# Performance work log

Hardware: AMD Instinct MI355X
Metric: run time of the kernel (lower is better)

## Reference

```python
import jax, jax.numpy as jnp
import numpy as np

ATOM_FDIM = 35
BOND_FDIM = 5
MAX_NB = 10
HIDDEN = 128
DEPTH = 6
A = 131072   # total atoms
B = 262144   # total directed bonds
M = 32768    # tree messages (row 0 is the zero pad vector, as in the torch code)
N_MOLS = 4096


def setup_inputs() -> dict:
    key = jax.random.key(0)
    ks = jax.random.split(key, 9)
    atom_feats = jax.random.uniform(ks[0], (A, ATOM_FDIM), dtype=jnp.float32)
    bond_feats = jax.random.uniform(ks[1], (B, ATOM_FDIM + BOND_FDIM), dtype=jnp.float32)
    tree_message = jax.random.normal(ks[2], (M, HIDDEN), dtype=jnp.float32)
    tree_message = tree_message.at[0].set(0.0)  # all_mess[0] = zeros padding
    atom_graph = jax.random.randint(ks[3], (A, MAX_NB), 0, M + B)
    bond_graph = jax.random.randint(ks[4], (B, MAX_NB), 0, M + B)
    s = 1.0 / np.sqrt(HIDDEN)
    W_i = jax.random.uniform(ks[5], (HIDDEN, ATOM_FDIM + BOND_FDIM), jnp.float32, -s, s)
    W_h = jax.random.uniform(ks[6], (HIDDEN, HIDDEN), jnp.float32, -s, s)
    W_o = jax.random.uniform(ks[7], (HIDDEN, ATOM_FDIM + HIDDEN), jnp.float32, -s, s)
    b_o = jax.random.uniform(ks[8], (HIDDEN,), jnp.float32, -s, s)
    return {"atom_feats": atom_feats, "bond_feats": bond_feats,
            "tree_message": tree_message, "atom_graph": atom_graph,
            "bond_graph": bond_graph, "n_mols": N_MOLS,
            "W_i": W_i, "W_h": W_h, "W_o": W_o, "b_o": b_o}


def reference(atom_feats, bond_feats, tree_message, atom_graph, bond_graph,
              n_mols, W_i, W_h, W_o, b_o):
    # h0 = ReLU(W_i @ bond_feats): [B, H]
    h0 = jax.nn.relu(jnp.einsum('bf,hf->bh', bond_feats, W_i))
    graph_message = h0
    for _ in range(DEPTH - 1):
        message = jnp.concatenate([tree_message, graph_message], axis=0)  # [M+B, H]
        nei = jnp.take(message, bond_graph, axis=0).sum(axis=1)           # [B, H]
        graph_message = jax.nn.relu(h0 + jnp.einsum('bh,gh->bg', nei, W_h))
    message = jnp.concatenate([tree_message, graph_message], axis=0)
    nei_a = jnp.take(message, atom_graph, axis=0).sum(axis=1)             # [A, H]
    atom_in = jnp.concatenate([atom_feats, nei_a], axis=1)                # [A, F+H]
    atom_hiddens = jax.nn.relu(jnp.einsum('af,hf->ah', atom_in, W_o) + b_o)
    # per-molecule mean over equal-size contiguous scopes
    atoms_per_mol = A // n_mols
    mol_ids = jnp.arange(A) // atoms_per_mol
    mol_vecs = jax.ops.segment_sum(atom_hiddens, mol_ids, num_segments=n_mols)
    return mol_vecs / atoms_per_mol
```

## Files before the change

### kernel.cpp

```cpp
#include <hip/hip_runtime.h>

#define H       128
#define MAXNB   10
#define M_TREE  32768
#define NBOND   262144
#define NATOM   131072
#define FATOM   35
#define FBOND   40
#define FOUT    163
#define KPAD    192
#define NMOLS   4096
#define APM     32
#define TB      64
#define TA      64

typedef __bf16 bf16x8 __attribute__((ext_vector_type(8)));
typedef float  f32x4  __attribute__((ext_vector_type(4)));
typedef unsigned int u32x4 __attribute__((ext_vector_type(4)));
typedef unsigned int u32x2 __attribute__((ext_vector_type(2)));

__device__ __forceinline__ unsigned short f32_to_bf16(float f) {
  unsigned int u = __float_as_uint(f);
  u += 0x7FFFu + ((u >> 16) & 1u);
  return (unsigned short)(u >> 16);
}
__device__ __forceinline__ float bf16u_to_f32(unsigned short h) {
  return __uint_as_float(((unsigned int)h) << 16);
}
__device__ __forceinline__ unsigned int bfpair_addrelu(unsigned int a, unsigned int h) {
  float a0 = __uint_as_float(a << 16), a1 = __uint_as_float(a & 0xFFFF0000u);
  float h0v = __uint_as_float(h << 16), h1v = __uint_as_float(h & 0xFFFF0000u);
  float r0 = fmaxf(a0 + h0v, 0.f), r1 = fmaxf(a1 + h1v, 0.f);
  return ((unsigned int)f32_to_bf16(r1) << 16) | (unsigned int)f32_to_bf16(r0);
}

__global__ __launch_bounds__(256) void prep(const float* __restrict__ tm,
                                            const float* __restrict__ wh,
                                            const float* __restrict__ wo,
                                            const float* __restrict__ wi,
                                            unsigned short* __restrict__ tmsg,
                                            unsigned short* __restrict__ whb,
                                            unsigned short* __restrict__ wob,
                                            unsigned short* __restrict__ wib) {
  const int blk = blockIdx.x;
  if (blk < 4096) {
    int i = (blk * 256 + threadIdx.x) * 4;
    f32x4 v = __builtin_nontemporal_load((const f32x4*)(tm + i));
    u32x2 p;
    p.x = (unsigned int)f32_to_bf16(v.x) | ((unsigned int)f32_to_bf16(v.y) << 16);
    p.y = (unsigned int)f32_to_bf16(v.z) | ((unsigned int)f32_to_bf16(v.w) << 16);
    *(u32x2*)(tmsg + i) = p;
    return;
  }
  int j = (blk - 4096) * 256 + threadIdx.x;
  const int n2 = H * H;
  const int n3 = H * KPAD;
  const int n4 = H * 64;
  if (j < n2) { whb[j] = f32_to_bf16(wh[j]); return; }
  int k = j - n2;
  if (k < n3) {
    int g = k / KPAD, kk = k - g * KPAD;
    float v = 0.f;
    if (kk < 35)                   v = wo[g * FOUT + kk];
    else if (kk >= 36 && kk < 164) v = wo[g * FOUT + kk - 1];
    wob[k] = f32_to_bf16(v);
    return;
  }
  int m = k - n3;
  if (m < n4) {
    int g = m / 64, kk = m - g * 64;
    wib[m] = (kk < FBOND) ? f32_to_bf16(wi[g * FBOND + kk]) : (unsigned short)0;
  }
}

__global__ __launch_bounds__(256, 3) void wi_gemm(const float* __restrict__ bond_feats,
                                                  const unsigned short* __restrict__ wib,
                                                  unsigned short* __restrict__ h0) {
  __shared__ unsigned short sF[128][72];
  const int t = threadIdx.x;
  const int lane = t & 63;
  const int wave = t >> 6;
  const int n16 = lane & 15;
  const int quad = lane >> 4;
  const int b0 = blockIdx.x * 128;

#pragma unroll
  for (int c = 0; c < 5; ++c) {
    int q = c * 256 + t;
    f32x4 v = __builtin_nontemporal_load((const f32x4*)(bond_feats + (size_t)b0 * FBOND + q * 4));
    int flat = q * 4;
    int row = flat / 40, col = flat - row * 40;
    u32x2 p;
    p.x = (unsigned int)f32_to_bf16(v.x) | ((unsigned int)f32_to_bf16(v.y) << 16);
    p.y = (unsigned int)f32_to_bf16(v.z) | ((unsigned int)f32_to_bf16(v.w) << 16);
    *(u32x2*)&sF[row][col] = p;
  }
  for (int i = t; i < 128 * 24; i += 256) {
    int b = i / 24, c = 40 + i - b * 24;
    sF[b][c] = 0;
  }
  bf16x8 Bf[2][2];
#pragma unroll
  for (int kt = 0; kt < 2; ++kt)
#pragma unroll
    for (int nt = 0; nt < 2; ++nt)
      Bf[kt][nt] = *(const bf16x8*)(wib + ((wave * 2 + nt) * 16 + n16) * 64 + kt * 32 + quad * 8);
  __syncthreads();

  f32x4 acc[8][2];
  f32x4 zero = {0.f, 0.f, 0.f, 0.f};
#pragma unroll
  for (int mt = 0; mt < 8; ++mt) { acc[mt][0] = zero; acc[mt][1] = zero; }
#pragma unroll
  for (int kt = 0; kt < 2; ++kt)
#pragma unroll
    for (int mt = 0; mt < 8; ++mt) {
      bf16x8 av = *(const bf16x8*)&sF[mt * 16 + n16][kt * 32 + quad * 8];
      acc[mt][0] = __builtin_amdgcn_mfma_f32_16x16x32_bf16(av, Bf[kt][0], acc[mt][0], 0, 0, 0);
      acc[mt][1] = __builtin_amdgcn_mfma_f32_16x16x32_bf16(av, Bf[kt][1], acc[mt][1], 0, 0, 0);
    }
#pragma unroll
  for (int mt = 0; mt < 8; ++mt)
#pragma unroll
    for (int nt = 0; nt < 2; ++nt) {
      const int col = (wave * 2 + nt) * 16 + n16;
#pragma unroll
      for (int r = 0; r < 4; ++r) {
        const int b = b0 + mt * 16 + quad * 4 + r;
        h0[b * H + col] = f32_to_bf16(fmaxf(acc[mt][nt][r], 0.f));
      }
    }
}

__global__ __launch_bounds__(256, 6) void mp_step(const unsigned short* __restrict__ gm_in,
                                                  unsigned short* __restrict__ gm_out,
                                                  const unsigned short* __restrict__ h0,
                                                  const unsigned short* __restrict__ tmsg,
                                                  const int* __restrict__ bond_graph,
                                                  const unsigned short* __restrict__ whb) {
  __shared__ unsigned short snei[TB][136];
  __shared__ int sBG[TB * MAXNB];
  const int t = threadIdx.x;
  const int lane = t & 63;
  const int wave = t >> 6;
  const int n16 = lane & 15;
  const int quad = lane >> 4;
  const int b0 = blockIdx.x * TB;

  for (int i = t; i < TB * MAXNB; i += 256) sBG[i] = bond_graph[b0 * MAXNB + i];
  __syncthreads();

  const unsigned short* gsh = gm_in - (size_t)M_TREE * H;
  for (int lb = wave * 4; lb < TB; lb += 16) {
    unsigned int u[4][MAXNB];
#pragma unroll
    for (int p = 0; p < 4; ++p) {
      const int* ig = &sBG[(lb + p) * MAXNB];
#pragma unroll
      for (int j = 0; j < MAXNB; ++j) {
        int idx = __builtin_amdgcn_readfirstlane(ig[j]);
        const unsigned short* r = ((idx < M_TREE) ? tmsg : gsh) + (size_t)idx * H;
        u[p][j] = *(const unsigned int*)(r + 2 * lane);
      }
    }
#pragma unroll
    for (int p = 0; p < 4; ++p) {
      float a0 = 0.f, a1 = 0.f;
#pragma unroll
      for (int j = 0; j < MAXNB; ++j) {
        a0 += __uint_as_float(u[p][j] << 16);
        a1 += __uint_as_float(u[p][j] & 0xFFFF0000u);
      }
      unsigned int packed = ((unsigned int)f32_to_bf16(a1) << 16) | (unsigned int)f32_to_bf16(a0);
      *(unsigned int*)&snei[lb + p][2 * lane] = packed;
    }
  }

  bf16x8 Bf[4][2];
#pragma unroll
  for (int kt = 0; kt < 4; ++kt)
#pragma unroll
    for (int nt = 0; nt < 2; ++nt)
      Bf[kt][nt] = *(const bf16x8*)(whb + ((wave * 2 + nt) * 16 + n16) * H + kt * 32 + quad * 8);
  __syncthreads();

  f32x4 acc[4][2];
  f32x4 zero = {0.f, 0.f, 0.f, 0.f};
#pragma unroll
  for (int mt = 0; mt < 4; ++mt) { acc[mt][0] = zero; acc[mt][1] = zero; }
#pragma unroll
  for (int kt = 0; kt < 4; ++kt)
#pragma unroll
    for (int mt = 0; mt < 4; ++mt) {
      bf16x8 av = *(const bf16x8*)&snei[mt * 16 + n16][kt * 32 + quad * 8];
      acc[mt][0] = __builtin_amdgcn_mfma_f32_16x16x32_bf16(av, Bf[kt][0], acc[mt][0], 0, 0, 0);
      acc[mt][1] = __builtin_amdgcn_mfma_f32_16x16x32_bf16(av, Bf[kt][1], acc[mt][1], 0, 0, 0);
    }
  __syncthreads();

#pragma unroll
  for (int mt = 0; mt < 4; ++mt)
#pragma unroll
    for (int nt = 0; nt < 2; ++nt) {
      const int col = (wave * 2 + nt) * 16 + n16;
#pragma unroll
      for (int r = 0; r < 4; ++r)
        snei[mt * 16 + quad * 4 + r][col] = f32_to_bf16(acc[mt][nt][r]);
    }
  __syncthreads();

  const size_t gbase = (size_t)b0 * H;
#pragma unroll
  for (int c = 0; c < 4; ++c) {
    int fl = c * 256 + t;
    int row = fl >> 4;
    int col = (fl & 15) * 8;
    u32x4 a4 = *(const u32x4*)&snei[row][col];
    u32x4 h4 = *(const u32x4*)(h0 + gbase + (size_t)row * H + col);
    u32x4 o4;
    o4.x = bfpair_addrelu(a4.x, h4.x);
    o4.y = bfpair_addrelu(a4.y, h4.y);
    o4.z = bfpair_addrelu(a4.z, h4.z);
    o4.w = bfpair_addrelu(a4.w, h4.w);
    *(u32x4*)(gm_out + gbase + (size_t)row * H + col) = o4;
  }
}

__global__ __launch_bounds__(256, 5) void readout(const float* __restrict__ atom_feats,
                                                  const unsigned short* __restrict__ gm,
                                                  const unsigned short* __restrict__ tmsg,
                                                  const int* __restrict__ atom_graph,
                                                  const unsigned short* __restrict__ wob,
                                                  const float* __restrict__ b_o,
                                                  float* __restrict__ out) {
  __shared__ unsigned short sA[TA][200];
  __shared__ int sAG[TA * MAXNB];
  const int t = threadIdx.x;
  const int lane = t & 63;
  const int wave = t >> 6;
  const int n16 = lane & 15;
  const int quad = lane >> 4;
  const int blk = blockIdx.x;
  const int abase = blk * TA;

  for (int i = t; i < TA * MAXNB; i += 256)
    sAG[i] = __builtin_nontemporal_load(atom_graph + abase * MAXNB + i);
  for (int i = t; i < TA * FATOM; i += 256) {
    int a = i / FATOM, f = i - a * FATOM;
    sA[a][f] = f32_to_bf16(__builtin_nontemporal_load(atom_feats + abase * FATOM + i));
  }
  if (t < TA) sA[t][35] = 0;
  for (int i = t; i < TA * 28; i += 256) {
    int a = i / 28, c = 164 + i - a * 28;
    sA[a][c] = 0;
  }
  __syncthreads();

  const unsigned short* gsh = gm - (size_t)M_TREE * H;
  for (int la = wave * 2; la < TA; la += 8) {
    unsigned int u[2][MAXNB];
#pragma unroll
    for (int p = 0; p < 2; ++p) {
      const int* ig = &sAG[(la + p) * MAXNB];
#pragma unroll
      for (int j = 0; j < MAXNB; ++j) {
        int idx = __builtin_amdgcn_readfirstlane(ig[j]);
        const unsigned short* r = ((idx < M_TREE) ? tmsg : gsh) + (size_t)idx * H;
        u[p][j] = *(const unsigned int*)(r + 2 * lane);
      }
    }
#pragma unroll
    for (int p = 0; p < 2; ++p) {
      float a0 = 0.f, a1 = 0.f;
#pragma unroll
      for (int j = 0; j < MAXNB; ++j) {
        a0 += __uint_as_float(u[p][j] << 16);
        a1 += __uint_as_float(u[p][j] & 0xFFFF0000u);
      }
      unsigned int packed = ((unsigned int)f32_to_bf16(a1) << 16) | (unsigned int)f32_to_bf16(a0);
      *(unsigned int*)&sA[la + p][36 + 2 * lane] = packed;
    }
  }

  bf16x8 Bf[6][2];
#pragma unroll
  for (int kt = 0; kt < 6; ++kt)
#pragma unroll
    for (int nt = 0; nt < 2; ++nt)
      Bf[kt][nt] = *(const bf16x8*)(wob + ((wave * 2 + nt) * 16 + n16) * KPAD + kt * 32 + quad * 8);
  __syncthreads();

  f32x4 acc[4][2];
  f32x4 zero = {0.f, 0.f, 0.f, 0.f};
#pragma unroll
  for (int mt = 0; mt < 4; ++mt) { acc[mt][0] = zero; acc[mt][1] = zero; }
#pragma unroll
  for (int kt = 0; kt < 6; ++kt)
#pragma unroll
    for (int mt = 0; mt < 4; ++mt) {
      bf16x8 av = *(const bf16x8*)&sA[mt * 16 + n16][kt * 32 + quad * 8];
      acc[mt][0] = __builtin_amdgcn_mfma_f32_16x16x32_bf16(av, Bf[kt][0], acc[mt][0], 0, 0, 0);
      acc[mt][1] = __builtin_amdgcn_mfma_f32_16x16x32_bf16(av, Bf[kt][1], acc[mt][1], 0, 0, 0);
    }

  float bo[2] = { b_o[(wave * 2) * 16 + n16], b_o[(wave * 2 + 1) * 16 + n16] };
  float part[2][2] = {{0.f,0.f},{0.f,0.f}};
#pragma unroll
  for (int mt = 0; mt < 4; ++mt)
#pragma unroll
    for (int nt = 0; nt < 2; ++nt)
#pragma unroll
      for (int r = 0; r < 4; ++r)
        part[mt >> 1][nt] += fmaxf(acc[mt][nt][r] + bo[nt], 0.f);
#pragma unroll
  for (int mol = 0; mol < 2; ++mol)
#pragma unroll
    for (int nt = 0; nt < 2; ++nt) {
      float p = part[mol][nt];
      p += __shfl_xor(p, 16);
      p += __shfl_xor(p, 32);
      if (lane < 16)
        out[(blk * 2 + mol) * H + (wave * 2 + nt) * 16 + lane] = p * (1.0f / APM);
    }
}

extern "C" void kernel_launch(void* const* d_in, const int* in_sizes, int n_in,
                              void* d_out, int out_size, void* d_ws, size_t ws_size,
                              hipStream_t stream) {
  (void)in_sizes; (void)n_in; (void)out_size; (void)ws_size;
  const float* atom_feats   = (const float*)d_in[0];
  const float* bond_feats   = (const float*)d_in[1];
  const float* tree_message = (const float*)d_in[2];
  const int*   atom_graph   = (const int*)d_in[3];
  const int*   bond_graph   = (const int*)d_in[4];
  const float* W_i = (const float*)d_in[6];
  const float* W_h = (const float*)d_in[7];
  const float* W_o = (const float*)d_in[8];
  const float* b_o = (const float*)d_in[9];
  float* out = (float*)d_out;

  char* ws = (char*)d_ws;
  unsigned short* tmsg = (unsigned short*)(ws);
  unsigned short* whb  = (unsigned short*)(ws + 8388608);
  unsigned short* wob  = (unsigned short*)(ws + 8421376);
  unsigned short* wib  = (unsigned short*)(ws + 8470528);
  unsigned short* h0   = (unsigned short*)(ws + 8486912);
  unsigned short* gm0  = (unsigned short*)(ws + 75595776);
  unsigned short* gm1  = (unsigned short*)(ws + 142704640);

  prep<<<4288, 256, 0, stream>>>(tree_message, W_h, W_o, W_i, tmsg, whb, wob, wib);
  wi_gemm<<<NBOND / 128, 256, 0, stream>>>(bond_feats, wib, h0);
  mp_step<<<NBOND / TB, 256, 0, stream>>>(h0,  gm0, h0, tmsg, bond_graph, whb);
  mp_step<<<NBOND / TB, 256, 0, stream>>>(gm0, gm1, h0, tmsg, bond_graph, whb);
  mp_step<<<NBOND / TB, 256, 0, stream>>>(gm1, gm0, h0, tmsg, bond_graph, whb);
  mp_step<<<NBOND / TB, 256, 0, stream>>>(gm0, gm1, h0, tmsg, bond_graph, whb);
  mp_step<<<NBOND / TB, 256, 0, stream>>>(gm1, gm0, h0, tmsg, bond_graph, whb);
  readout<<<NATOM / TA, 256, 0, stream>>>(atom_feats, gm0, tmsg, atom_graph, wob, b_o, out);
}
```

Measured before the change: 747.2 us.

## Precompute constant tree-message term once and gather only graph messages per step

The W_h product is linear, so the tree-message part of the neighbour sum never changes across steps. It is now computed once inside wi_gemm and folded with h0 into a precomputed bias (hT). Each message-passing step then gathers only graph messages: a remapped bond_graph sends every tree index to a zeroed pad row, which removes the per-neighbour tree/graph pointer select and the scattered tree-row reads. Nontemporal loads and stores are added for streamed buffers. The cost is an extra bf16 rounding of the folded bias, an extra index-remap pass in prep, and more work in wi_gemm.

New measurement: 812.6 us. +8.8%, slower.

```diff
diff --git a/kernel.cpp b/kernel.cpp
--- a/kernel.cpp
+++ b/kernel.cpp
@@ -18,6 +18,7 @@
 typedef float  f32x4  __attribute__((ext_vector_type(4)));
 typedef unsigned int u32x4 __attribute__((ext_vector_type(4)));
 typedef unsigned int u32x2 __attribute__((ext_vector_type(2)));
+typedef int          i32x4 __attribute__((ext_vector_type(4)));
 
 __device__ __forceinline__ unsigned short f32_to_bf16(float f) {
   unsigned int u = __float_as_uint(f);
@@ -38,10 +39,14 @@
                                             const float* __restrict__ wh,
                                             const float* __restrict__ wo,
                                             const float* __restrict__ wi,
+                                            const int* __restrict__ bond_graph,
                                             unsigned short* __restrict__ tmsg,
                                             unsigned short* __restrict__ whb,
                                             unsigned short* __restrict__ wob,
-                                            unsigned short* __restrict__ wib) {
+                                            unsigned short* __restrict__ wib,
+                                            int* __restrict__ bg2,
+                                            unsigned short* __restrict__ bufA,
+                                            unsigned short* __restrict__ gm0) {
   const int blk = blockIdx.x;
   if (blk < 4096) {
     int i = (blk * 256 + threadIdx.x) * 4;
@@ -52,31 +57,54 @@
     *(u32x2*)(tmsg + i) = p;
     return;
   }
-  int j = (blk - 4096) * 256 + threadIdx.x;
-  const int n2 = H * H;
-  const int n3 = H * KPAD;
-  const int n4 = H * 64;
-  if (j < n2) { whb[j] = f32_to_bf16(wh[j]); return; }
-  int k = j - n2;
-  if (k < n3) {
-    int g = k / KPAD, kk = k - g * KPAD;
-    float v = 0.f;
-    if (kk < 35)                   v = wo[g * FOUT + kk];
-    else if (kk >= 36 && kk < 164) v = wo[g * FOUT + kk - 1];
-    wob[k] = f32_to_bf16(v);
+  if (blk < 4288) {
+    int j = (blk - 4096) * 256 + threadIdx.x;
+    const int n2 = H * H;
+    const int n3 = H * KPAD;
+    const int n4 = H * 64;
+    if (j < n2) { whb[j] = f32_to_bf16(wh[j]); return; }
+    int k = j - n2;
+    if (k < n3) {
+      int g = k / KPAD, kk = k - g * KPAD;
+      float v = 0.f;
+      if (kk < 35)                   v = wo[g * FOUT + kk];
+      else if (kk >= 36 && kk < 164) v = wo[g * FOUT + kk - 1];
+      wob[k] = f32_to_bf16(v);
+      return;
+    }
+    int m = k - n3;
+    if (m < n4) {
+      int g = m / 64, kk = m - g * 64;
+      wib[m] = (kk < FBOND) ? f32_to_bf16(wi[g * FBOND + kk]) : (unsigned short)0;
+    }
     return;
   }
-  int m = k - n3;
-  if (m < n4) {
-    int g = m / 64, kk = m - g * 64;
-    wib[m] = (kk < FBOND) ? f32_to_bf16(wi[g * FBOND + kk]) : (unsigned short)0;
+  if (blk < 4288 + 2560) {
+    int q = ((blk - 4288) * 256 + threadIdx.x) * 4;
+    i32x4 v = __builtin_nontemporal_load((const i32x4*)(bond_graph + q));
+    i32x4 o;
+    o.x = (v.x < M_TREE) ? NBOND : (v.x - M_TREE);
+    o.y = (v.y < M_TREE) ? NBOND : (v.y - M_TREE);
+    o.z = (v.z < M_TREE) ? NBOND : (v.z - M_TREE);
+    o.w = (v.w < M_TREE) ? NBOND : (v.w - M_TREE);
+    __builtin_nontemporal_store(o, (i32x4*)(bg2 + q));
+    return;
+  }
+  if (threadIdx.x < 128) {
+    bufA[(size_t)NBOND * H + threadIdx.x] = 0;
+    gm0 [(size_t)NBOND * H + threadIdx.x] = 0;
   }
 }
 
 __global__ __launch_bounds__(256, 3) void wi_gemm(const float* __restrict__ bond_feats,
                                                   const unsigned short* __restrict__ wib,
-                                                  unsigned short* __restrict__ h0) {
-  __shared__ unsigned short sF[128][72];
+                                                  const unsigned short* __restrict__ whb,
+                                                  const unsigned short* __restrict__ tmsg,
+                                                  const int* __restrict__ bond_graph,
+                                                  unsigned short* __restrict__ h0,
+                                                  unsigned short* __restrict__ hT) {
+  __shared__ unsigned short sT[128][136];
+  __shared__ int sBG[128 * MAXNB];
   const int t = threadIdx.x;
   const int lane = t & 63;
   const int wave = t >> 6;
@@ -93,18 +121,21 @@
     u32x2 p;
     p.x = (unsigned int)f32_to_bf16(v.x) | ((unsigned int)f32_to_bf16(v.y) << 16);
     p.y = (unsigned int)f32_to_bf16(v.z) | ((unsigned int)f32_to_bf16(v.w) << 16);
-    *(u32x2*)&sF[row][col] = p;
+    *(u32x2*)&sT[row][col] = p;
   }
   for (int i = t; i < 128 * 24; i += 256) {
     int b = i / 24, c = 40 + i - b * 24;
-    sF[b][c] = 0;
-  }
-  bf16x8 Bf[2][2];
+    sT[b][c] = 0;
+  }
+  for (int i = t; i < 128 * MAXNB; i += 256)
+    sBG[i] = __builtin_nontemporal_load(bond_graph + (size_t)b0 * MAXNB + i);
+
+  bf16x8 Bi[2][2];
 #pragma unroll
   for (int kt = 0; kt < 2; ++kt)
 #pragma unroll
     for (int nt = 0; nt < 2; ++nt)
-      Bf[kt][nt] = *(const bf16x8*)(wib + ((wave * 2 + nt) * 16 + n16) * 64 + kt * 32 + quad * 8);
+      Bi[kt][nt] = *(const bf16x8*)(wib + ((wave * 2 + nt) * 16 + n16) * 64 + kt * 32 + quad * 8);
   __syncthreads();
 
   f32x4 acc[8][2];
@@ -115,9 +146,9 @@
   for (int kt = 0; kt < 2; ++kt)
 #pragma unroll
     for (int mt = 0; mt < 8; ++mt) {
-      bf16x8 av = *(const bf16x8*)&sF[mt * 16 + n16][kt * 32 + quad * 8];
-      acc[mt][0] = __builtin_amdgcn_mfma_f32_16x16x32_bf16(av, Bf[kt][0], acc[mt][0], 0, 0, 0);
-      acc[mt][1] = __builtin_amdgcn_mfma_f32_16x16x32_bf16(av, Bf[kt][1], acc[mt][1], 0, 0, 0);
+      bf16x8 av = *(const bf16x8*)&sT[mt * 16 + n16][kt * 32 + quad * 8];
+      acc[mt][0] = __builtin_amdgcn_mfma_f32_16x16x32_bf16(av, Bi[kt][0], acc[mt][0], 0, 0, 0);
+      acc[mt][1] = __builtin_amdgcn_mfma_f32_16x16x32_bf16(av, Bi[kt][1], acc[mt][1], 0, 0, 0);
     }
 #pragma unroll
   for (int mt = 0; mt < 8; ++mt)
@@ -127,16 +158,64 @@
 #pragma unroll
       for (int r = 0; r < 4; ++r) {
         const int b = b0 + mt * 16 + quad * 4 + r;
-        h0[b * H + col] = f32_to_bf16(fmaxf(acc[mt][nt][r], 0.f));
-      }
-    }
+        __builtin_nontemporal_store(f32_to_bf16(fmaxf(acc[mt][nt][r], 0.f)), &h0[(size_t)b * H + col]);
+      }
+    }
+  __syncthreads();
+
+  for (int lb = wave * 4; lb < 128; lb += 16) {
+#pragma unroll
+    for (int p = 0; p < 4; ++p) {
+      const int* ig = &sBG[(lb + p) * MAXNB];
+      float a0 = 0.f, a1 = 0.f;
+#pragma unroll
+      for (int j = 0; j < MAXNB; ++j) {
+        int idx = __builtin_amdgcn_readfirstlane(ig[j]);
+        if (idx < M_TREE) {
+          unsigned int u = *(const unsigned int*)(tmsg + (size_t)idx * H + 2 * lane);
+          a0 += __uint_as_float(u << 16);
+          a1 += __uint_as_float(u & 0xFFFF0000u);
+        }
+      }
+      unsigned int packed = ((unsigned int)f32_to_bf16(a1) << 16) | (unsigned int)f32_to_bf16(a0);
+      *(unsigned int*)&sT[lb + p][2 * lane] = packed;
+    }
+  }
+
+  bf16x8 Bh[4][2];
+#pragma unroll
+  for (int kt = 0; kt < 4; ++kt)
+#pragma unroll
+    for (int nt = 0; nt < 2; ++nt)
+      Bh[kt][nt] = *(const bf16x8*)(whb + ((wave * 2 + nt) * 16 + n16) * H + kt * 32 + quad * 8);
+  __syncthreads();
+
+#pragma unroll
+  for (int mt = 0; mt < 8; ++mt) {
+    f32x4 acch[2] = {zero, zero};
+#pragma unroll
+    for (int kt = 0; kt < 4; ++kt) {
+      bf16x8 av = *(const bf16x8*)&sT[mt * 16 + n16][kt * 32 + quad * 8];
+      acch[0] = __builtin_amdgcn_mfma_f32_16x16x32_bf16(av, Bh[kt][0], acch[0], 0, 0, 0);
+      acch[1] = __builtin_amdgcn_mfma_f32_16x16x32_bf16(av, Bh[kt][1], acch[1], 0, 0, 0);
+    }
+#pragma unroll
+    for (int nt = 0; nt < 2; ++nt) {
+      const int col = (wave * 2 + nt) * 16 + n16;
+#pragma unroll
+      for (int r = 0; r < 4; ++r) {
+        const int b = b0 + mt * 16 + quad * 4 + r;
+        float hr = fmaxf(acc[mt][nt][r], 0.f);
+        __builtin_nontemporal_store(f32_to_bf16(hr + acch[nt][r]), &hT[(size_t)b * H + col]);
+      }
+    }
+  }
 }
 
 __global__ __launch_bounds__(256, 6) void mp_step(const unsigned short* __restrict__ gm_in,
                                                   unsigned short* __restrict__ gm_out,
-                                                  const unsigned short* __restrict__ h0,
-                                                  const unsigned short* __restrict__ tmsg,
-                                                  const int* __restrict__ bond_graph,
+                                                  const unsigned short* __restrict__ hT,
+                                                  const int* __restrict__ bg2,
                                                   const unsigned short* __restrict__ whb) {
   __shared__ unsigned short snei[TB][136];
   __shared__ int sBG[TB * MAXNB];
@@ -147,10 +226,10 @@
   const int quad = lane >> 4;
   const int b0 = blockIdx.x * TB;
 
-  for (int i = t; i < TB * MAXNB; i += 256) sBG[i] = bond_graph[b0 * MAXNB + i];
-  __syncthreads();
-
-  const unsigned short* gsh = gm_in - (size_t)M_TREE * H;
+  for (int i = t; i < TB * MAXNB; i += 256)
+    sBG[i] = __builtin_nontemporal_load(bg2 + (size_t)b0 * MAXNB + i);
+  __syncthreads();
+
   for (int lb = wave * 4; lb < TB; lb += 16) {
     unsigned int u[4][MAXNB];
 #pragma unroll
@@ -159,8 +238,7 @@
 #pragma unroll
       for (int j = 0; j < MAXNB; ++j) {
         int idx = __builtin_amdgcn_readfirstlane(ig[j]);
-        const unsigned short* r = ((idx < M_TREE) ? tmsg : gsh) + (size_t)idx * H;
-        u[p][j] = *(const unsigned int*)(r + 2 * lane);
+        u[p][j] = *(const unsigned int*)(gm_in + (size_t)idx * H + 2 * lane);
       }
     }
 #pragma unroll
@@ -216,13 +294,13 @@
     int row = fl >> 4;
     int col = (fl & 15) * 8;
     u32x4 a4 = *(const u32x4*)&snei[row][col];
-    u32x4 h4 = *(const u32x4*)(h0 + gbase + (size_t)row * H + col);
+    u32x4 h4 = __builtin_nontemporal_load((const u32x4*)(hT + gbase + (size_t)row * H + col));
     u32x4 o4;
     o4.x = bfpair_addrelu(a4.x, h4.x);
     o4.y = bfpair_addrelu(a4.y, h4.y);
     o4.z = bfpair_addrelu(a4.z, h4.z);
     o4.w = bfpair_addrelu(a4.w, h4.w);
-    *(u32x4*)(gm_out + gbase + (size_t)row * H + col) = o4;
+    __builtin_nontemporal_store(o4, (u32x4*)(gm_out + gbase + (size_t)row * H + col));
   }
 }
 
@@ -344,16 +422,18 @@
   unsigned short* whb  = (unsigned short*)(ws + 8388608);
   unsigned short* wob  = (unsigned short*)(ws + 8421376);
   unsigned short* wib  = (unsigned short*)(ws + 8470528);
-  unsigned short* h0   = (unsigned short*)(ws + 8486912);
-  unsigned short* gm0  = (unsigned short*)(ws + 75595776);
-  unsigned short* gm1  = (unsigned short*)(ws + 142704640);
-
-  prep<<<4288, 256, 0, stream>>>(tree_message, W_h, W_o, W_i, tmsg, whb, wob, wib);
-  wi_gemm<<<NBOND / 128, 256, 0, stream>>>(bond_feats, wib, h0);
-  mp_step<<<NBOND / TB, 256, 0, stream>>>(h0,  gm0, h0, tmsg, bond_graph, whb);
-  mp_step<<<NBOND / TB, 256, 0, stream>>>(gm0, gm1, h0, tmsg, bond_graph, whb);
-  mp_step<<<NBOND / TB, 256, 0, stream>>>(gm1, gm0, h0, tmsg, bond_graph, whb);
-  mp_step<<<NBOND / TB, 256, 0, stream>>>(gm0, gm1, h0, tmsg, bond_graph, whb);
-  mp_step<<<NBOND / TB, 256, 0, stream>>>(gm1, gm0, h0, tmsg, bond_graph, whb);
+  int*            bg2  = (int*)           (ws + 8486912);
+  unsigned short* bufA = (unsigned short*)(ws + 18972672);
+  unsigned short* gm0  = (unsigned short*)(ws + 86081792);
+  unsigned short* hT   = (unsigned short*)(ws + 153190912);
+
+  prep<<<6849, 256, 0, stream>>>(tree_message, W_h, W_o, W_i, bond_graph,
+                                 tmsg, whb, wob, wib, bg2, bufA, gm0);
+  wi_gemm<<<NBOND / 128, 256, 0, stream>>>(bond_feats, wib, whb, tmsg, bond_graph, bufA, hT);
+  mp_step<<<NBOND / TB, 256, 0, stream>>>(bufA, gm0, hT, bg2, whb);
+  mp_step<<<NBOND / TB, 256, 0, stream>>>(gm0, bufA, hT, bg2, whb);
+  mp_step<<<NBOND / TB, 256, 0, stream>>>(bufA, gm0, hT, bg2, whb);
+  mp_step<<<NBOND / TB, 256, 0, stream>>>(gm0, bufA, hT, bg2, whb);
+  mp_step<<<NBOND / TB, 256, 0, stream>>>(bufA, gm0, hT, bg2, whb);
   readout<<<NATOM / TA, 256, 0, stream>>>(atom_feats, gm0, tmsg, atom_graph, wob, b_o, out);
 }
```

## Use contiguous tree+graph message buffers with 16-byte vector gathers and dot2 accumulation

Applied to the files above, without the earlier changes.

Stores the tree messages in front of each ping-pong graph message buffer, so a single base pointer indexes the concatenated message table and the per-neighbor tmsg/gm branch and readfirstlane go away. Each gather now has 16 lanes per bond loading 16-byte chunks, with 4 bonds per wave instruction, instead of one bond per wave with 4-byte loads. Accumulation switches to v_dot2_f32_bf16. In exchange, the tree messages are written twice and h0 is duplicated into the A buffer, and the readout padding layout is shifted to align columns to 8.

Result: no change. 753.7 us (+0.9%).

```diff
diff --git a/kernel.cpp b/kernel.cpp
--- a/kernel.cpp
+++ b/kernel.cpp
@@ -9,7 +9,6 @@
 #define FBOND   40
 #define FOUT    163
 #define KPAD    192
-#define NMOLS   4096
 #define APM     32
 #define TB      64
 #define TA      64
@@ -18,14 +17,13 @@
 typedef float  f32x4  __attribute__((ext_vector_type(4)));
 typedef unsigned int u32x4 __attribute__((ext_vector_type(4)));
 typedef unsigned int u32x2 __attribute__((ext_vector_type(2)));
+typedef int          i32x4 __attribute__((ext_vector_type(4)));
+typedef int          i32x2 __attribute__((ext_vector_type(2)));
 
 __device__ __forceinline__ unsigned short f32_to_bf16(float f) {
   unsigned int u = __float_as_uint(f);
   u += 0x7FFFu + ((u >> 16) & 1u);
   return (unsigned short)(u >> 16);
-}
-__device__ __forceinline__ float bf16u_to_f32(unsigned short h) {
-  return __uint_as_float(((unsigned int)h) << 16);
 }
 __device__ __forceinline__ unsigned int bfpair_addrelu(unsigned int a, unsigned int h) {
   float a0 = __uint_as_float(a << 16), a1 = __uint_as_float(a & 0xFFFF0000u);
@@ -33,12 +31,20 @@
   float r0 = fmaxf(a0 + h0v, 0.f), r1 = fmaxf(a1 + h1v, 0.f);
   return ((unsigned int)f32_to_bf16(r1) << 16) | (unsigned int)f32_to_bf16(r0);
 }
+__device__ __forceinline__ void bfdot_acc(unsigned int u, float& a0, float& a1) {
+  asm("v_dot2_f32_bf16 %0, %1, %2, %0" : "+v"(a0) : "v"(u), "v"(0x00003F80u));
+  asm("v_dot2_f32_bf16 %0, %1, %2, %0" : "+v"(a1) : "v"(u), "v"(0x3F800000u));
+}
+__device__ __forceinline__ unsigned int pack2(float a0, float a1) {
+  return ((unsigned int)f32_to_bf16(a1) << 16) | (unsigned int)f32_to_bf16(a0);
+}
 
 __global__ __launch_bounds__(256) void prep(const float* __restrict__ tm,
                                             const float* __restrict__ wh,
                                             const float* __restrict__ wo,
                                             const float* __restrict__ wi,
-                                            unsigned short* __restrict__ tmsg,
+                                            unsigned short* __restrict__ tA,
+                                            unsigned short* __restrict__ tB,
                                             unsigned short* __restrict__ whb,
                                             unsigned short* __restrict__ wob,
                                             unsigned short* __restrict__ wib) {
@@ -49,7 +55,8 @@
     u32x2 p;
     p.x = (unsigned int)f32_to_bf16(v.x) | ((unsigned int)f32_to_bf16(v.y) << 16);
     p.y = (unsigned int)f32_to_bf16(v.z) | ((unsigned int)f32_to_bf16(v.w) << 16);
-    *(u32x2*)(tmsg + i) = p;
+    *(u32x2*)(tA + i) = p;
+    *(u32x2*)(tB + i) = p;
     return;
   }
   int j = (blk - 4096) * 256 + threadIdx.x;
@@ -62,7 +69,7 @@
     int g = k / KPAD, kk = k - g * KPAD;
     float v = 0.f;
     if (kk < 35)                   v = wo[g * FOUT + kk];
-    else if (kk >= 36 && kk < 164) v = wo[g * FOUT + kk - 1];
+    else if (kk >= 40 && kk < 168) v = wo[g * FOUT + kk - 5];
     wob[k] = f32_to_bf16(v);
     return;
   }
@@ -75,7 +82,8 @@
 
 __global__ __launch_bounds__(256, 3) void wi_gemm(const float* __restrict__ bond_feats,
                                                   const unsigned short* __restrict__ wib,
-                                                  unsigned short* __restrict__ h0) {
+                                                  unsigned short* __restrict__ h0,
+                                                  unsigned short* __restrict__ h0A) {
   __shared__ unsigned short sF[128][72];
   const int t = threadIdx.x;
   const int lane = t & 63;
@@ -127,19 +135,20 @@
 #pragma unroll
       for (int r = 0; r < 4; ++r) {
         const int b = b0 + mt * 16 + quad * 4 + r;
-        h0[b * H + col] = f32_to_bf16(fmaxf(acc[mt][nt][r], 0.f));
+        unsigned short hv = f32_to_bf16(fmaxf(acc[mt][nt][r], 0.f));
+        h0 [(size_t)b * H + col] = hv;
+        h0A[(size_t)b * H + col] = hv;
       }
     }
 }
 
-__global__ __launch_bounds__(256, 6) void mp_step(const unsigned short* __restrict__ gm_in,
+__global__ __launch_bounds__(256, 6) void mp_step(const unsigned short* __restrict__ src,
                                                   unsigned short* __restrict__ gm_out,
                                                   const unsigned short* __restrict__ h0,
-                                                  const unsigned short* __restrict__ tmsg,
                                                   const int* __restrict__ bond_graph,
                                                   const unsigned short* __restrict__ whb) {
   __shared__ unsigned short snei[TB][136];
-  __shared__ int sBG[TB * MAXNB];
+  __shared__ int sBG[TB][16];
   const int t = threadIdx.x;
   const int lane = t & 63;
   const int wave = t >> 6;
@@ -147,33 +156,42 @@
   const int quad = lane >> 4;
   const int b0 = blockIdx.x * TB;
 
-  for (int i = t; i < TB * MAXNB; i += 256) sBG[i] = bond_graph[b0 * MAXNB + i];
-  __syncthreads();
-
-  const unsigned short* gsh = gm_in - (size_t)M_TREE * H;
-  for (int lb = wave * 4; lb < TB; lb += 16) {
-    unsigned int u[4][MAXNB];
-#pragma unroll
-    for (int p = 0; p < 4; ++p) {
-      const int* ig = &sBG[(lb + p) * MAXNB];
-#pragma unroll
-      for (int j = 0; j < MAXNB; ++j) {
-        int idx = __builtin_amdgcn_readfirstlane(ig[j]);
-        const unsigned short* r = ((idx < M_TREE) ? tmsg : gsh) + (size_t)idx * H;
-        u[p][j] = *(const unsigned int*)(r + 2 * lane);
-      }
-    }
-#pragma unroll
-    for (int p = 0; p < 4; ++p) {
-      float a0 = 0.f, a1 = 0.f;
-#pragma unroll
-      for (int j = 0; j < MAXNB; ++j) {
-        a0 += __uint_as_float(u[p][j] << 16);
-        a1 += __uint_as_float(u[p][j] & 0xFFFF0000u);
-      }
-      unsigned int packed = ((unsigned int)f32_to_bf16(a1) << 16) | (unsigned int)f32_to_bf16(a0);
-      *(unsigned int*)&snei[lb + p][2 * lane] = packed;
-    }
+  for (int i = t; i < TB * MAXNB; i += 256) {
+    int b = i / MAXNB, j = i - b * MAXNB;
+    sBG[b][j] = bond_graph[(size_t)b0 * MAXNB + i];
+  }
+  __syncthreads();
+
+  const unsigned char* sp = (const unsigned char*)src;
+  const unsigned int so = (unsigned int)n16 * 16u;
+  for (int it = 0; it < 4; ++it) {
+    const int lb = wave * 16 + it * 4 + quad;
+    i32x4 iv0 = *(const i32x4*)&sBG[lb][0];
+    i32x4 iv1 = *(const i32x4*)&sBG[lb][4];
+    i32x2 iv2 = *(const i32x2*)&sBG[lb][8];
+    unsigned int ix[10] = {(unsigned int)iv0.x, (unsigned int)iv0.y, (unsigned int)iv0.z,
+                           (unsigned int)iv0.w, (unsigned int)iv1.x, (unsigned int)iv1.y,
+                           (unsigned int)iv1.z, (unsigned int)iv1.w, (unsigned int)iv2.x,
+                           (unsigned int)iv2.y};
+    u32x4 u4[10];
+#pragma unroll
+    for (int j = 0; j < MAXNB; ++j)
+      u4[j] = *(const u32x4*)(sp + (ix[j] * 256u + so));
+    float ac0 = 0.f, ac1 = 0.f, ac2 = 0.f, ac3 = 0.f;
+    float ac4 = 0.f, ac5 = 0.f, ac6 = 0.f, ac7 = 0.f;
+#pragma unroll
+    for (int j = 0; j < MAXNB; ++j) {
+      bfdot_acc(u4[j].x, ac0, ac1);
+      bfdot_acc(u4[j].y, ac2, ac3);
+      bfdot_acc(u4[j].z, ac4, ac5);
+      bfdot_acc(u4[j].w, ac6, ac7);
+    }
+    u32x4 o;
+    o.x = pack2(ac0, ac1);
+    o.y = pack2(ac2, ac3);
+    o.z = pack2(ac4, ac5);
+    o.w = pack2(ac6, ac7);
+    *(u32x4*)&snei[lb][n16 * 8] = o;
   }
 
   bf16x8 Bf[4][2];
@@ -227,14 +245,13 @@
 }
 
 __global__ __launch_bounds__(256, 5) void readout(const float* __restrict__ atom_feats,
-                                                  const unsigned short* __restrict__ gm,
-                                                  const unsigned short* __restrict__ tmsg,
+                                                  const unsigned short* __restrict__ src,
                                                   const int* __restrict__ atom_graph,
                                                   const unsigned short* __restrict__ wob,
                                                   const float* __restrict__ b_o,
                                                   float* __restrict__ out) {
-  __shared__ unsigned short sA[TA][200];
-  __shared__ int sAG[TA * MAXNB];
+  __shared__ unsigned short sA[TA][208];
+  __shared__ int sAG[TA][16];
   const int t = threadIdx.x;
   const int lane = t & 63;
   const int wave = t >> 6;
@@ -243,43 +260,54 @@
   const int blk = blockIdx.x;
   const int abase = blk * TA;
 
-  for (int i = t; i < TA * MAXNB; i += 256)
-    sAG[i] = __builtin_nontemporal_load(atom_graph + abase * MAXNB + i);
+  for (int i = t; i < TA * MAXNB; i += 256) {
+    int a = i / MAXNB, j = i - a * MAXNB;
+    sAG[a][j] = __builtin_nontemporal_load(atom_graph + (size_t)abase * MAXNB + i);
+  }
   for (int i = t; i < TA * FATOM; i += 256) {
     int a = i / FATOM, f = i - a * FATOM;
-    sA[a][f] = f32_to_bf16(__builtin_nontemporal_load(atom_feats + abase * FATOM + i));
-  }
-  if (t < TA) sA[t][35] = 0;
-  for (int i = t; i < TA * 28; i += 256) {
-    int a = i / 28, c = 164 + i - a * 28;
+    sA[a][f] = f32_to_bf16(__builtin_nontemporal_load(atom_feats + (size_t)abase * FATOM + i));
+  }
+  if (t < TA) {
+#pragma unroll
+    for (int c = 35; c < 40; ++c) sA[t][c] = 0;
+  }
+  for (int i = t; i < TA * 24; i += 256) {
+    int a = i / 24, c = 168 + i - a * 24;
     sA[a][c] = 0;
   }
   __syncthreads();
 
-  const unsigned short* gsh = gm - (size_t)M_TREE * H;
-  for (int la = wave * 2; la < TA; la += 8) {
-    unsigned int u[2][MAXNB];
-#pragma unroll
-    for (int p = 0; p < 2; ++p) {
-      const int* ig = &sAG[(la + p) * MAXNB];
-#pragma unroll
-      for (int j = 0; j < MAXNB; ++j) {
-        int idx = __builtin_amdgcn_readfirstlane(ig[j]);
-        const unsigned short* r = ((idx < M_TREE) ? tmsg : gsh) + (size_t)idx * H;
-        u[p][j] = *(const unsigned int*)(r + 2 * lane);
-      }
-    }
-#pragma unroll
-    for (int p = 0; p < 2; ++p) {
-      float a0 = 0.f, a1 = 0.f;
-#pragma unroll
-      for (int j = 0; j < MAXNB; ++j) {
-        a0 += __uint_as_float(u[p][j] << 16);
-        a1 += __uint_as_float(u[p][j] & 0xFFFF0000u);
-      }
-      unsigned int packed = ((unsigned int)f32_to_bf16(a1) << 16) | (unsigned int)f32_to_bf16(a0);
-      *(unsigned int*)&sA[la + p][36 + 2 * lane] = packed;
-    }
+  const unsigned char* sp = (const unsigned char*)src;
+  const unsigned int so = (unsigned int)n16 * 16u;
+  for (int it = 0; it < 4; ++it) {
+    const int la = wave * 16 + it * 4 + quad;
+    i32x4 iv0 = *(const i32x4*)&sAG[la][0];
+    i32x4 iv1 = *(const i32x4*)&sAG[la][4];
+    i32x2 iv2 = *(const i32x2*)&sAG[la][8];
+    unsigned int ix[10] = {(unsigned int)iv0.x, (unsigned int)iv0.y, (unsigned int)iv0.z,
+                           (unsigned int)iv0.w, (unsigned int)iv1.x, (unsigned int)iv1.y,
+                           (unsigned int)iv1.z, (unsigned int)iv1.w, (unsigned int)iv2.x,
+                           (unsigned int)iv2.y};
+    u32x4 u4[10];
+#pragma unroll
+    for (int j = 0; j < MAXNB; ++j)
+      u4[j] = *(const u32x4*)(sp + (ix[j] * 256u + so));
+    float ac0 = 0.f, ac1 = 0.f, ac2 = 0.f, ac3 = 0.f;
+    float ac4 = 0.f, ac5 = 0.f, ac6 = 0.f, ac7 = 0.f;
+#pragma unroll
+    for (int j = 0; j < MAXNB; ++j) {
+      bfdot_acc(u4[j].x, ac0, ac1);
+      bfdot_acc(u4[j].y, ac2, ac3);
+      bfdot_acc(u4[j].z, ac4, ac5);
+      bfdot_acc(u4[j].w, ac6, ac7);
+    }
+    u32x4 o;
+    o.x = pack2(ac0, ac1);
+    o.y = pack2(ac2, ac3);
+    o.z = pack2(ac4, ac5);
+    o.w = pack2(ac6, ac7);
+    *(u32x4*)&sA[la][40 + n16 * 8] = o;
   }
 
   bf16x8 Bf[6][2];
@@ -340,20 +368,21 @@
   float* out = (float*)d_out;
 
   char* ws = (char*)d_ws;
-  unsigned short* tmsg = (unsigned short*)(ws);
-  unsigned short* whb  = (unsigned short*)(ws + 8388608);
-  unsigned short* wob  = (unsigned short*)(ws + 8421376);
-  unsigned short* wib  = (unsigned short*)(ws + 8470528);
-  unsigned short* h0   = (unsigned short*)(ws + 8486912);
-  unsigned short* gm0  = (unsigned short*)(ws + 75595776);
-  unsigned short* gm1  = (unsigned short*)(ws + 142704640);
-
-  prep<<<4288, 256, 0, stream>>>(tree_message, W_h, W_o, W_i, tmsg, whb, wob, wib);
-  wi_gemm<<<NBOND / 128, 256, 0, stream>>>(bond_feats, wib, h0);
-  mp_step<<<NBOND / TB, 256, 0, stream>>>(h0,  gm0, h0, tmsg, bond_graph, whb);
-  mp_step<<<NBOND / TB, 256, 0, stream>>>(gm0, gm1, h0, tmsg, bond_graph, whb);
-  mp_step<<<NBOND / TB, 256, 0, stream>>>(gm1, gm0, h0, tmsg, bond_graph, whb);
-  mp_step<<<NBOND / TB, 256, 0, stream>>>(gm0, gm1, h0, tmsg, bond_graph, whb);
-  mp_step<<<NBOND / TB, 256, 0, stream>>>(gm1, gm0, h0, tmsg, bond_graph, whb);
-  readout<<<NATOM / TA, 256, 0, stream>>>(atom_feats, gm0, tmsg, atom_graph, wob, b_o, out);
-}
+  unsigned short* A    = (unsigned short*)(ws);
+  unsigned short* B    = (unsigned short*)(ws + 75497472);
+  unsigned short* h0   = (unsigned short*)(ws + 150994944);
+  unsigned short* whb  = (unsigned short*)(ws + 218103808);
+  unsigned short* wob  = (unsigned short*)(ws + 218136576);
+  unsigned short* wib  = (unsigned short*)(ws + 218185728);
+  unsigned short* Atail = A + (size_t)M_TREE * H;
+  unsigned short* Btail = B + (size_t)M_TREE * H;
+
+  prep<<<4288, 256, 0, stream>>>(tree_message, W_h, W_o, W_i, A, B, whb, wob, wib);
+  wi_gemm<<<NBOND / 128, 256, 0, stream>>>(bond_feats, wib, h0, Atail);
+  mp_step<<<NBOND / TB, 256, 0, stream>>>(A, Btail, h0, bond_graph, whb);
+  mp_step<<<NBOND / TB, 256, 0, stream>>>(B, Atail, h0, bond_graph, whb);
+  mp_step<<<NBOND / TB, 256, 0, stream>>>(A, Btail, h0, bond_graph, whb);
+  mp_step<<<NBOND / TB, 256, 0, stream>>>(B, Atail, h0, bond_graph, whb);
+  mp_step<<<NBOND / TB, 256, 0, stream>>>(A, Btail, h0, bond_graph, whb);
+  readout<<<NATOM / TA, 256, 0, stream>>>(atom_feats, B, atom_graph, wob, b_o, out);
+}
```
